# Optimization experiments

Measured on AMD Instinct MI355X. Metric: run time of the kernel, lower is better.

Reference implementation:

```python
import jax, jax.numpy as jnp
import numpy as np

B, A, NB, BOND = 256, 100, 10, 110
AF, BF, H, DEPTH = 82, 6, 300, 3

def setup_inputs() -> dict:
    key = jax.random.key(0)
    ks = jax.random.split(key, 16)
    atom_feats = jax.random.normal(ks[0], (B, A, AF), dtype=jnp.float32)
    bond_feats = jax.random.normal(ks[1], (B, BOND, BF), dtype=jnp.float32)
    ag_b = jax.random.randint(ks[2], (B, A, NB, 1), 0, B, dtype=jnp.int32)
    ag_a = jax.random.randint(ks[3], (B, A, NB, 1), 0, A, dtype=jnp.int32)
    atom_graph = jnp.concatenate([ag_b, ag_a], axis=-1)
    bg_b = jax.random.randint(ks[4], (B, A, NB, 1), 0, B, dtype=jnp.int32)
    bg_e = jax.random.randint(ks[5], (B, A, NB, 1), 0, BOND, dtype=jnp.int32)
    bond_graph = jnp.concatenate([bg_b, bg_e], axis=-1)
    num_nbs = jax.random.randint(ks[6], (B, A), 0, NB + 1, dtype=jnp.int32)
    n_atoms = jax.random.randint(ks[7], (B,), 50, A + 1, dtype=jnp.int32)
    n_atoms = n_atoms.at[0].set(A)  # padding must equal n_atoms.max()
    sc = lambda i, o: (2.0 / (i + o)) ** 0.5
    w_fc1 = jax.random.normal(ks[8], (AF, H), dtype=jnp.float32) * sc(AF, H)
    w_nei = jax.random.normal(ks[9], (H + BF, H), dtype=jnp.float32) * sc(H + BF, H)
    b_nei = jnp.zeros((H,), dtype=jnp.float32)
    w_atom = jax.random.normal(ks[10], (2 * H, H), dtype=jnp.float32) * sc(2 * H, H)
    b_atom = jnp.zeros((H,), dtype=jnp.float32)
    w2a = jax.random.normal(ks[11], (H, H), dtype=jnp.float32) * sc(H, H)
    w2b = jax.random.normal(ks[12], (BF, H), dtype=jnp.float32) * sc(BF, H)
    w_fc2 = jax.random.normal(ks[13], (H, H), dtype=jnp.float32) * sc(H, H)
    return dict(atom_feats=atom_feats, bond_feats=bond_feats, w_fc1=w_fc1,
                w_nei=w_nei, b_nei=b_nei, w_atom=w_atom, b_atom=b_atom,
                w2a=w2a, w2b=w2b, w_fc2=w_fc2, atom_graph=atom_graph,
                bond_graph=bond_graph, num_nbs=num_nbs, n_atoms=n_atoms)

def reference(atom_feats, bond_feats, w_fc1, w_nei, b_nei, w_atom, b_atom,
              w2a, w2b, w_fc2, atom_graph, bond_graph, num_nbs, n_atoms):
    h = jax.nn.relu(atom_feats @ w_fc1)                      # [B,A,H]
    bondnei = bond_feats[bond_graph[..., 0], bond_graph[..., 1]]  # [B,A,NB,BF]
    mask_neis = (num_nbs[..., None] > jnp.arange(NB, dtype=jnp.int32))[..., None]
    mask_atoms = (n_atoms[:, None] > jnp.arange(A, dtype=jnp.int32))[..., None]
    for i in range(DEPTH):
        atomnei = h[atom_graph[..., 0], atom_graph[..., 1]]  # [B,A,NB,H]
        if i + 1 == DEPTH:
            nei = (atomnei @ w2a) * (bondnei @ w2b)          # [B,A,NB,H]
            nei = jnp.where(mask_neis, nei, 0.0).sum(-2)     # [B,A,H]
            local = (h @ w_fc2) * nei
            local = jnp.where(mask_atoms, local, 0.0)
        else:
            nei = jax.nn.relu(jnp.concatenate([atomnei, bondnei], -1) @ w_nei + b_nei)
            nei = jnp.where(mask_neis, nei, 0.0).sum(-2)
            h = jax.nn.relu(jnp.concatenate([h, nei], -1) @ w_atom + b_atom)
    return local
```

## Files before the change

kernel.cpp:

```cpp
#include <hip/hip_runtime.h>

#define B_    256
#define A_    100
#define NB_   10
#define BOND_ 110
#define AF_   82
#define BF_   6
#define H_    300
#define NP_   320
#define MA_   (B_ * A_)
#define MB_   (B_ * BOND_)
#define KP300 320
#define KP82  96

typedef __attribute__((ext_vector_type(8))) short short8;
typedef __attribute__((ext_vector_type(4))) float f32x4;

__device__ __forceinline__ ushort f2bf(float v) {
    union { float f; unsigned u; } x; x.f = v;
    unsigned r = x.u + 0x7fffu + ((x.u >> 16) & 1u);
    return (ushort)(r >> 16);
}
__device__ __forceinline__ float bf2f(ushort h) {
    union { float f; unsigned u; } x; x.u = ((unsigned)h) << 16;
    return x.f;
}

__device__ __forceinline__ void gload16(const void* g, void* l) {
    __builtin_amdgcn_global_load_lds(
        (const __attribute__((address_space(1))) void*)g,
        (__attribute__((address_space(3))) void*)l, 16, 0, 0);
}

template<bool DUAL, bool BIAS, bool RELU, int OUTMODE>
__global__ __launch_bounds__(256, 2) void mgemm_k(
    const ushort* __restrict__ aH, const ushort* __restrict__ aL,
    const ushort* __restrict__ fH, const ushort* __restrict__ fL,
    const ushort* __restrict__ aH2, const ushort* __restrict__ aL2,
    const ushort* __restrict__ fH2, const ushort* __restrict__ fL2,
    int KP,
    const float* __restrict__ bias,
    const float* __restrict__ E,
    const int*   __restrict__ n_atoms,
    ushort* __restrict__ oHi, ushort* __restrict__ oLo,
    float*  __restrict__ oF)
{
    __shared__ char lds[3 * 8192];
    const int tid  = threadIdx.x;
    const int lane = tid & 63;
    const int l16  = lane & 15;
    const int kg   = lane >> 4;
    const int w    = tid >> 6;
    const int rowbase = blockIdx.x * 64;

    const int nks   = KP >> 5;
    const int total = (DUAL ? 2 : 1) * nks;

    const size_t srow = (size_t)(rowbase + (tid >> 2)) * KP;
    const int    sch  = (tid & 3) * 8;

    auto stage = [&](int t) {
        int pass = (DUAL && t >= nks) ? 1 : 0;
        int ks   = t - (pass ? nks : 0);
        const ushort* SH = pass ? aH2 : aH;
        const ushort* SL = pass ? aL2 : aL;
        char* dst = (char*)lds + (t % 3) * 8192 + (tid & 192) * 16;
        gload16(SH + srow + ks * 32 + sch, dst);
        gload16(SL + srow + ks * 32 + sch, dst + 4096);
    };

    f32x4 acc[4][5] = {};
    const int aoff = l16 * 64 + kg * 16;

    stage(0);
    for (int tk = 0; tk < total; ++tk) {
        short8 bh[5], bl[5];
        {
            int pass = (DUAL && tk >= nks) ? 1 : 0;
            int ks   = tk - (pass ? nks : 0);
            const ushort* FHp = pass ? fH2 : fH;
            const ushort* FLp = pass ? fL2 : fL;
            size_t base = ((size_t)ks * 20 + w * 5) * 512 + (size_t)lane * 8;
            #pragma unroll
            for (int c = 0; c < 5; ++c) {
                bh[c] = *(const short8*)(FHp + base + c * 512);
                bl[c] = *(const short8*)(FLp + base + c * 512);
            }
        }
        if (tk + 1 < total) stage(tk + 1);

        if (tk + 1 < total) { asm volatile("s_waitcnt vmcnt(2)" ::: "memory"); }
        else                { asm volatile("s_waitcnt vmcnt(0)" ::: "memory"); }
        __builtin_amdgcn_s_barrier();
        __builtin_amdgcn_sched_barrier(0);

        const char* ab = (const char*)lds + (tk % 3) * 8192;
        #pragma unroll
        for (int rt = 0; rt < 4; ++rt) {
            short8 ah = *(const short8*)(ab +        rt * 1024 + aoff);
            short8 al = *(const short8*)(ab + 4096 + rt * 1024 + aoff);
            #pragma unroll
            for (int c = 0; c < 5; ++c) {
                acc[rt][c] = __builtin_amdgcn_mfma_f32_16x16x32_bf16(ah, bh[c], acc[rt][c], 0, 0, 0);
                acc[rt][c] = __builtin_amdgcn_mfma_f32_16x16x32_bf16(al, bh[c], acc[rt][c], 0, 0, 0);
                acc[rt][c] = __builtin_amdgcn_mfma_f32_16x16x32_bf16(ah, bl[c], acc[rt][c], 0, 0, 0);
            }
        }
    }

    float biasv[5];
    #pragma unroll
    for (int c = 0; c < 5; ++c) {
        int col = w * 80 + c * 16 + l16;
        biasv[c] = (BIAS && col < H_) ? bias[col] : 0.f;
    }
    #pragma unroll
    for (int rt = 0; rt < 4; ++rt) {
        #pragma unroll
        for (int c = 0; c < 5; ++c) {
            const int col = w * 80 + c * 16 + l16;
            #pragma unroll
            for (int r = 0; r < 4; ++r) {
                const int row = rowbase + rt * 16 + kg * 4 + r;
                float v = acc[rt][c][r];
                if (BIAS) v += biasv[c];
                if (RELU) v = fmaxf(v, 0.f);
                if (OUTMODE == 0) {
                    ushort hi = f2bf(v);
                    ushort lo = f2bf(v - bf2f(hi));
                    size_t o = (size_t)row * NP_ + col;
                    oHi[o] = hi; oLo[o] = lo;
                } else if (OUTMODE == 1) {
                    oF[(size_t)row * NP_ + col] = v;
                } else {
                    if (col < H_) {
                        v *= E[(size_t)row * NP_ + col];
                        int b = row / A_;
                        int a = row - b * A_;
                        if (a >= n_atoms[b]) v = 0.f;
                        oF[(size_t)row * H_ + col] = v;
                    }
                }
            }
        }
    }
}

__global__ __launch_bounds__(256) void conv_wfrag_k(
    const float* __restrict__ src, int K, int KP,
    ushort* __restrict__ dH, ushort* __restrict__ dL)
{
    int idx = blockIdx.x * 256 + threadIdx.x;
    int nwords = (KP >> 5) * 20 * 64;
    if (idx >= nwords) return;
    int lane = idx & 63;
    int t  = idx >> 6;
    int ct = t % 20;
    int ks = t / 20;
    int col = ct * 16 + (lane & 15);
    int k0  = ks * 32 + (lane >> 4) * 8;
    short8 hv, lv;
    #pragma unroll
    for (int j = 0; j < 8; ++j) {
        int k = k0 + j;
        float v = (col < H_ && k < K) ? src[(size_t)k * H_ + col] : 0.f;
        ushort h = f2bf(v);
        hv[j] = (short)h;
        lv[j] = (short)f2bf(v - bf2f(h));
    }
    *(short8*)(dH + (size_t)idx * 8) = hv;
    *(short8*)(dL + (size_t)idx * 8) = lv;
}

__global__ __launch_bounds__(256) void conv_af_k(
    const float* __restrict__ src, ushort* __restrict__ dhi, ushort* __restrict__ dlo)
{
    int idx = blockIdx.x * 256 + threadIdx.x;
    if (idx >= MA_ * KP82) return;
    int row = idx / KP82, k = idx - row * KP82;
    float v = (k < AF_) ? src[(size_t)row * AF_ + k] : 0.f;
    ushort hi = f2bf(v);
    dhi[idx] = hi;
    dlo[idx] = f2bf(v - bf2f(hi));
}

__global__ __launch_bounds__(256) void bondmm_k(
    const float* __restrict__ bf, const float* __restrict__ wmat,
    const float* __restrict__ bias, float* __restrict__ out)
{
    int idx = blockIdx.x * 256 + threadIdx.x;
    if (idx >= MB_ * 80) return;
    int row = idx / 80, c4 = idx - row * 80;
    float4 s = make_float4(0.f, 0.f, 0.f, 0.f);
    if (c4 < 75) {
        int col = c4 * 4;
        if (bias) s = *(const float4*)(bias + col);
        #pragma unroll
        for (int k = 0; k < 6; ++k) {
            float b = bf[(size_t)row * 6 + k];
            float4 wv = *(const float4*)(wmat + (size_t)k * H_ + col);
            s.x = fmaf(b, wv.x, s.x); s.y = fmaf(b, wv.y, s.y);
            s.z = fmaf(b, wv.z, s.z); s.w = fmaf(b, wv.w, s.w);
        }
    }
    *(float4*)(out + (size_t)row * NP_ + c4 * 4) = s;
}

__global__ __launch_bounds__(256) void agg_relu_k(
    const float* __restrict__ hw, const float* __restrict__ bwn,
    const int* __restrict__ ag, const int* __restrict__ bg,
    const int* __restrict__ num_nbs,
    ushort* __restrict__ neiH, ushort* __restrict__ neiL)
{
    int idx = blockIdx.x * 256 + threadIdx.x;
    if (idx >= MA_ * 80) return;
    int ba = idx / 80, c4 = idx - ba * 80;
    int nn = num_nbs[ba];
    const int* agp = ag + (size_t)ba * NB_ * 2;
    const int* bgp = bg + (size_t)ba * NB_ * 2;
    float4 s = make_float4(0.f, 0.f, 0.f, 0.f);
    for (int n = 0; n < nn; ++n) {
        int arow = agp[2*n] * A_    + agp[2*n+1];
        int brow = bgp[2*n] * BOND_ + bgp[2*n+1];
        float4 hv = *(const float4*)(hw  + (size_t)arow * NP_ + c4 * 4);
        float4 bv = *(const float4*)(bwn + (size_t)brow * NP_ + c4 * 4);
        s.x += fmaxf(hv.x + bv.x, 0.f); s.y += fmaxf(hv.y + bv.y, 0.f);
        s.z += fmaxf(hv.z + bv.z, 0.f); s.w += fmaxf(hv.w + bv.w, 0.f);
    }
    size_t o = (size_t)ba * NP_ + c4 * 4;
    ushort4 hi, lo;
    hi.x = f2bf(s.x); lo.x = f2bf(s.x - bf2f(hi.x));
    hi.y = f2bf(s.y); lo.y = f2bf(s.y - bf2f(hi.y));
    hi.z = f2bf(s.z); lo.z = f2bf(s.z - bf2f(hi.z));
    hi.w = f2bf(s.w); lo.w = f2bf(s.w - bf2f(hi.w));
    *(ushort4*)(neiH + o) = hi;
    *(ushort4*)(neiL + o) = lo;
}

__global__ __launch_bounds__(256) void agg_prod_k(
    const float* __restrict__ hw2, const float* __restrict__ bw2,
    const int* __restrict__ ag, const int* __restrict__ bg,
    const int* __restrict__ num_nbs, float* __restrict__ neiF)
{
    int idx = blockIdx.x * 256 + threadIdx.x;
    if (idx >= MA_ * 80) return;
    int ba = idx / 80, c4 = idx - ba * 80;
    int nn = num_nbs[ba];
    const int* agp = ag + (size_t)ba * NB_ * 2;
    const int* bgp = bg + (size_t)ba * NB_ * 2;
    float4 s = make_float4(0.f, 0.f, 0.f, 0.f);
    for (int n = 0; n < nn; ++n) {
        int arow = agp[2*n] * A_    + agp[2*n+1];
        int brow = bgp[2*n] * BOND_ + bgp[2*n+1];
        float4 hv = *(const float4*)(hw2 + (size_t)arow * NP_ + c4 * 4);
        float4 bv = *(const float4*)(bw2 + (size_t)brow * NP_ + c4 * 4);
        s.x = fmaf(hv.x, bv.x, s.x); s.y = fmaf(hv.y, bv.y, s.y);
        s.z = fmaf(hv.z, bv.z, s.z); s.w = fmaf(hv.w, bv.w, s.w);
    }
    *(float4*)(neiF + (size_t)ba * NP_ + c4 * 4) = s;
}

extern "C" void kernel_launch(void* const* d_in, const int* in_sizes, int n_in,
                              void* d_out, int out_size, void* d_ws, size_t ws_size,
                              hipStream_t stream)
{
    const float* atom_feats = (const float*)d_in[0];
    const float* bond_feats = (const float*)d_in[1];
    const float* w_fc1      = (const float*)d_in[2];
    const float* w_nei      = (const float*)d_in[3];
    const float* b_nei      = (const float*)d_in[4];
    const float* w_atom     = (const float*)d_in[5];
    const float* b_atom     = (const float*)d_in[6];
    const float* w2a        = (const float*)d_in[7];
    const float* w2b        = (const float*)d_in[8];
    const float* w_fc2      = (const float*)d_in[9];
    const int*   atom_graph = (const int*)d_in[10];
    const int*   bond_graph = (const int*)d_in[11];
    const int*   num_nbs    = (const int*)d_in[12];
    const int*   n_atoms    = (const int*)d_in[13];
    float* out = (float*)d_out;
    (void)in_sizes; (void)n_in; (void)out_size; (void)ws_size;

    const size_t SZ_H16 = (size_t)MA_ * NP_ * 2;
    const size_t SZ_HF  = (size_t)MA_ * NP_ * 4;
    const size_t SZ_BWN = (size_t)MB_ * NP_ * 4;
    const size_t SZ_AF  = (size_t)MA_ * KP82 * 2;
    const size_t SZ_WT  = (size_t)NP_ * KP300 * 2;
    const size_t SZ_WT1 = (size_t)NP_ * KP82 * 2;
    char* p = (char*)d_ws;
    ushort* hA_h = (ushort*)p; p += SZ_H16;
    ushort* hA_l = (ushort*)p; p += SZ_H16;
    ushort* hB_h = (ushort*)p; p += SZ_H16;
    ushort* hB_l = (ushort*)p; p += SZ_H16;
    ushort* nei_h = (ushort*)p; p += SZ_H16;
    ushort* nei_l = (ushort*)p; p += SZ_H16;
    float* hwF = (float*)p; p += SZ_HF;
    float* bwn = (float*)p; p += SZ_BWN;
    ushort* af_h = (ushort*)p; p += SZ_AF;
    ushort* af_l = (ushort*)p; p += SZ_AF;
    ushort* wfc1_h = (ushort*)p; p += SZ_WT1;
    ushort* wfc1_l = (ushort*)p; p += SZ_WT1;
    ushort* wn1_h  = (ushort*)p; p += SZ_WT;
    ushort* wn1_l  = (ushort*)p; p += SZ_WT;
    ushort* wa1_h  = (ushort*)p; p += SZ_WT;
    ushort* wa1_l  = (ushort*)p; p += SZ_WT;
    ushort* wa2_h  = (ushort*)p; p += SZ_WT;
    ushort* wa2_l  = (ushort*)p; p += SZ_WT;
    ushort* w2a_h  = (ushort*)p; p += SZ_WT;
    ushort* w2a_l  = (ushort*)p; p += SZ_WT;
    ushort* wfc2_h = (ushort*)p; p += SZ_WT;
    ushort* wfc2_l = (ushort*)p; p += SZ_WT;
    float* neiF = (float*)hB_h;

    const dim3 blk(256);
    const dim3 gG(MA_ / 64);
    const int  aggG  = (MA_ * 80 + 255) / 256;
    const int  bondG = (MB_ * 80 + 255) / 256;
    const int  fw300 = ((KP300 >> 5) * 20 * 64 + 255) / 256;
    const int  fw96  = ((KP82  >> 5) * 20 * 64 + 255) / 256;

    conv_af_k<<<(MA_*KP82+255)/256, blk, 0, stream>>>(atom_feats, af_h, af_l);
    conv_wfrag_k<<<fw96,  blk, 0, stream>>>(w_fc1, AF_, KP82, wfc1_h, wfc1_l);
    conv_wfrag_k<<<fw300, blk, 0, stream>>>(w_nei,                 H_, KP300, wn1_h, wn1_l);
    conv_wfrag_k<<<fw300, blk, 0, stream>>>(w_atom,                H_, KP300, wa1_h, wa1_l);
    conv_wfrag_k<<<fw300, blk, 0, stream>>>(w_atom + (size_t)H_*H_, H_, KP300, wa2_h, wa2_l);
    conv_wfrag_k<<<fw300, blk, 0, stream>>>(w2a,                   H_, KP300, w2a_h, w2a_l);
    conv_wfrag_k<<<fw300, blk, 0, stream>>>(w_fc2,                 H_, KP300, wfc2_h, wfc2_l);

    bondmm_k<<<bondG, blk, 0, stream>>>(bond_feats, w_nei + (size_t)H_*H_, b_nei, bwn);

    mgemm_k<false,false,true,0><<<gG, blk, 0, stream>>>(
        af_h, af_l, wfc1_h, wfc1_l, nullptr,nullptr,nullptr,nullptr, KP82,
        nullptr, nullptr, nullptr, hA_h, hA_l, nullptr);

    ushort* hc_h = hA_h; ushort* hc_l = hA_l;
    ushort* hn_h = hB_h; ushort* hn_l = hB_l;
    for (int it = 0; it < 2; ++it) {
        mgemm_k<false,false,false,1><<<gG, blk, 0, stream>>>(
            hc_h, hc_l, wn1_h, wn1_l, nullptr,nullptr,nullptr,nullptr, KP300,
            nullptr, nullptr, nullptr, nullptr, nullptr, hwF);
        agg_relu_k<<<aggG, blk, 0, stream>>>(hwF, bwn, atom_graph, bond_graph, num_nbs, nei_h, nei_l);
        mgemm_k<true,true,true,0><<<gG, blk, 0, stream>>>(
            hc_h, hc_l, wa1_h, wa1_l, nei_h, nei_l, wa2_h, wa2_l, KP300,
            b_atom, nullptr, nullptr, hn_h, hn_l, nullptr);
        ushort* t;
        t = hc_h; hc_h = hn_h; hn_h = t;
        t = hc_l; hc_l = hn_l; hn_l = t;
    }

    bondmm_k<<<bondG, blk, 0, stream>>>(bond_feats, w2b, nullptr, bwn);
    mgemm_k<false,false,false,1><<<gG, blk, 0, stream>>>(
        hc_h, hc_l, w2a_h, w2a_l, nullptr,nullptr,nullptr,nullptr, KP300,
        nullptr, nullptr, nullptr, nullptr, nullptr, hwF);
    agg_prod_k<<<aggG, blk, 0, stream>>>(hwF, bwn, atom_graph, bond_graph, num_nbs, neiF);
    mgemm_k<false,false,false,2><<<gG, blk, 0, stream>>>(
        hc_h, hc_l, wfc2_h, wfc2_l, nullptr,nullptr,nullptr,nullptr, KP300,
        nullptr, neiF, n_atoms, nullptr, nullptr, out);
}
```

Baseline: 454.5 us.

## Enlarge GEMM row tile to 100 rows with 512-thread blocks and 4-stage pipeline

The bf16-split GEMM kernel now uses 512-thread blocks covering 100 rows (one molecule) per block. Eight waves are arranged as 2 row groups by 4 column groups, and the second row group handles only 3 row tiles. The A-tile staging becomes a 4-buffer LDS ring with double-buffered B fragments in registers and a two-step unrolled loop with explicit vmcnt waits, so weight fragment loads are reused across more rows and overlapped with MFMA work. The grid shrinks to 256 blocks. This risks lower occupancy from higher register and LDS use, and wastes work on padded row tiles.

```diff
diff --git a/kernel.cpp b/kernel.cpp
--- a/kernel.cpp
+++ b/kernel.cpp
@@ -13,6 +13,12 @@
 #define KP300 320
 #define KP82  96
 
+#define BM_     100
+#define BMST_   112
+#define PLANE_  7168
+#define BUFSZ_  14336
+#define DUMP_   57344
+
 typedef __attribute__((ext_vector_type(8))) short short8;
 typedef __attribute__((ext_vector_type(4))) float f32x4;
 
@@ -33,7 +39,7 @@
 }
 
 template<bool DUAL, bool BIAS, bool RELU, int OUTMODE>
-__global__ __launch_bounds__(256, 2) void mgemm_k(
+__global__ __launch_bounds__(512, 2) void mgemm_k(
     const ushort* __restrict__ aH, const ushort* __restrict__ aL,
     const ushort* __restrict__ fH, const ushort* __restrict__ fL,
     const ushort* __restrict__ aH2, const ushort* __restrict__ aL2,
@@ -45,100 +51,162 @@
     ushort* __restrict__ oHi, ushort* __restrict__ oLo,
     float*  __restrict__ oF)
 {
-    __shared__ char lds[3 * 8192];
+    __shared__ char lds[4 * BUFSZ_ + 2048];
     const int tid  = threadIdx.x;
     const int lane = tid & 63;
     const int l16  = lane & 15;
     const int kg   = lane >> 4;
     const int w    = tid >> 6;
-    const int rowbase = blockIdx.x * 64;
+    const int wr   = w >> 2;
+    const int wc   = w & 3;
+    const int nrt  = wr ? 3 : 4;
+    const int rowbase = blockIdx.x * BM_;
 
     const int nks   = KP >> 5;
     const int total = (DUAL ? 2 : 1) * nks;
 
-    const size_t srow = (size_t)(rowbase + (tid >> 2)) * KP;
-    const int    sch  = (tid & 3) * 8;
+    bool  spl[2], sdmp[2];
+    size_t ssoff[2];
+    int   sdoff[2];
+    #pragma unroll
+    for (int i = 0; i < 2; ++i) {
+        int s = 2 * w + i;
+        bool isdump = (s >= 14);
+        int se = isdump ? 0 : s;
+        int p  = (se >= 7) ? 1 : 0;
+        int t  = se - p * 7;
+        int row = t * 16 + (lane >> 2);
+        int grow = rowbase + row; if (grow >= MA_) grow = MA_ - 1;
+        spl[i]  = (p != 0);
+        sdmp[i] = isdump;
+        ssoff[i] = (size_t)grow * KP + (lane & 3) * 8;
+        sdoff[i] = isdump ? (DUMP_ + i * 1024) : (p * PLANE_ + t * 1024);
+    }
 
     auto stage = [&](int t) {
         int pass = (DUAL && t >= nks) ? 1 : 0;
         int ks   = t - (pass ? nks : 0);
-        const ushort* SH = pass ? aH2 : aH;
-        const ushort* SL = pass ? aL2 : aL;
-        char* dst = (char*)lds + (t % 3) * 8192 + (tid & 192) * 16;
-        gload16(SH + srow + ks * 32 + sch, dst);
-        gload16(SL + srow + ks * 32 + sch, dst + 4096);
+        const ushort* PH = pass ? aH2 : aH;
+        const ushort* PL = pass ? aL2 : aL;
+        char* bb = (char*)lds + (t & 3) * BUFSZ_;
+        #pragma unroll
+        for (int i = 0; i < 2; ++i) {
+            const ushort* src = (spl[i] ? PL : PH) + ssoff[i] + ks * 32;
+            char* dst = (sdmp[i] ? (char*)lds : bb) + sdoff[i];
+            gload16(src, dst);
+        }
     };
 
+    auto loadB = [&](int t, short8* bh, short8* bl) {
+        int pass = (DUAL && t >= nks) ? 1 : 0;
+        int ks   = t - (pass ? nks : 0);
+        const ushort* FHp = pass ? fH2 : fH;
+        const ushort* FLp = pass ? fL2 : fL;
+        size_t base = ((size_t)ks * 20 + wc * 5) * 512 + (size_t)lane * 8;
+        #pragma unroll
+        for (int c = 0; c < 5; ++c) {
+            bh[c] = *(const short8*)(FHp + base + c * 512);
+            bl[c] = *(const short8*)(FLp + base + c * 512);
+        }
+    };
+
     f32x4 acc[4][5] = {};
-    const int aoff = l16 * 64 + kg * 16;
+    const int ao = l16 * 64 + kg * 16;
+
+    auto mstep = [&](int t, const short8* bh, const short8* bl) {
+        const char* ab = (const char*)lds + (t & 3) * BUFSZ_ + wr * 4096;
+        #pragma unroll
+        for (int rt = 0; rt < 4; ++rt) {
+            if (rt < nrt) {
+                short8 ah = *(const short8*)(ab + rt * 1024 + ao);
+                short8 al = *(const short8*)(ab + PLANE_ + rt * 1024 + ao);
+                #pragma unroll
+                for (int c = 0; c < 5; ++c) {
+                    acc[rt][c] = __builtin_amdgcn_mfma_f32_16x16x32_bf16(ah, bh[c], acc[rt][c], 0, 0, 0);
+                    acc[rt][c] = __builtin_amdgcn_mfma_f32_16x16x32_bf16(al, bh[c], acc[rt][c], 0, 0, 0);
+                    acc[rt][c] = __builtin_amdgcn_mfma_f32_16x16x32_bf16(ah, bl[c], acc[rt][c], 0, 0, 0);
+                }
+            }
+        }
+    };
+
+    short8 bAh[5], bAl[5], bBh[5], bBl[5];
 
     stage(0);
-    for (int tk = 0; tk < total; ++tk) {
-        short8 bh[5], bl[5];
-        {
-            int pass = (DUAL && tk >= nks) ? 1 : 0;
-            int ks   = tk - (pass ? nks : 0);
-            const ushort* FHp = pass ? fH2 : fH;
-            const ushort* FLp = pass ? fL2 : fL;
-            size_t base = ((size_t)ks * 20 + w * 5) * 512 + (size_t)lane * 8;
-            #pragma unroll
-            for (int c = 0; c < 5; ++c) {
-                bh[c] = *(const short8*)(FHp + base + c * 512);
-                bl[c] = *(const short8*)(FLp + base + c * 512);
-            }
-        }
-        if (tk + 1 < total) stage(tk + 1);
-
-        if (tk + 1 < total) { asm volatile("s_waitcnt vmcnt(2)" ::: "memory"); }
-        else                { asm volatile("s_waitcnt vmcnt(0)" ::: "memory"); }
+    __builtin_amdgcn_sched_barrier(0);
+    loadB(0, bAh, bAl);
+    __builtin_amdgcn_sched_barrier(0);
+    if (1 < total) stage(1);
+    __builtin_amdgcn_sched_barrier(0);
+
+    for (int tk = 0; tk < total; tk += 2) {
+        if (tk + 2 < total) {
+            loadB(tk + 1, bBh, bBl);
+            __builtin_amdgcn_sched_barrier(0);
+            stage(tk + 2);
+            asm volatile("s_waitcnt vmcnt(14)" ::: "memory");
+        } else if (tk + 1 < total) {
+            loadB(tk + 1, bBh, bBl);
+            asm volatile("s_waitcnt vmcnt(12)" ::: "memory");
+        } else {
+            asm volatile("s_waitcnt vmcnt(0)" ::: "memory");
+        }
         __builtin_amdgcn_s_barrier();
         __builtin_amdgcn_sched_barrier(0);
-
-        const char* ab = (const char*)lds + (tk % 3) * 8192;
-        #pragma unroll
-        for (int rt = 0; rt < 4; ++rt) {
-            short8 ah = *(const short8*)(ab +        rt * 1024 + aoff);
-            short8 al = *(const short8*)(ab + 4096 + rt * 1024 + aoff);
-            #pragma unroll
-            for (int c = 0; c < 5; ++c) {
-                acc[rt][c] = __builtin_amdgcn_mfma_f32_16x16x32_bf16(ah, bh[c], acc[rt][c], 0, 0, 0);
-                acc[rt][c] = __builtin_amdgcn_mfma_f32_16x16x32_bf16(al, bh[c], acc[rt][c], 0, 0, 0);
-                acc[rt][c] = __builtin_amdgcn_mfma_f32_16x16x32_bf16(ah, bl[c], acc[rt][c], 0, 0, 0);
-            }
-        }
+        mstep(tk, bAh, bAl);
+        if (tk + 1 >= total) break;
+
+        if (tk + 3 < total) {
+            loadB(tk + 2, bAh, bAl);
+            __builtin_amdgcn_sched_barrier(0);
+            stage(tk + 3);
+            asm volatile("s_waitcnt vmcnt(14)" ::: "memory");
+        } else if (tk + 2 < total) {
+            loadB(tk + 2, bAh, bAl);
+            asm volatile("s_waitcnt vmcnt(12)" ::: "memory");
+        } else {
+            asm volatile("s_waitcnt vmcnt(0)" ::: "memory");
+        }
+        __builtin_amdgcn_s_barrier();
+        __builtin_amdgcn_sched_barrier(0);
+        mstep(tk + 1, bBh, bBl);
     }
 
     float biasv[5];
     #pragma unroll
     for (int c = 0; c < 5; ++c) {
-        int col = w * 80 + c * 16 + l16;
+        int col = wc * 80 + c * 16 + l16;
         biasv[c] = (BIAS && col < H_) ? bias[col] : 0.f;
     }
     #pragma unroll
     for (int rt = 0; rt < 4; ++rt) {
-        #pragma unroll
-        for (int c = 0; c < 5; ++c) {
-            const int col = w * 80 + c * 16 + l16;
+        if (rt < nrt) {
             #pragma unroll
-            for (int r = 0; r < 4; ++r) {
-                const int row = rowbase + rt * 16 + kg * 4 + r;
-                float v = acc[rt][c][r];
-                if (BIAS) v += biasv[c];
-                if (RELU) v = fmaxf(v, 0.f);
-                if (OUTMODE == 0) {
-                    ushort hi = f2bf(v);
-                    ushort lo = f2bf(v - bf2f(hi));
-                    size_t o = (size_t)row * NP_ + col;
-                    oHi[o] = hi; oLo[o] = lo;
-                } else if (OUTMODE == 1) {
-                    oF[(size_t)row * NP_ + col] = v;
-                } else {
-                    if (col < H_) {
-                        v *= E[(size_t)row * NP_ + col];
-                        int b = row / A_;
-                        int a = row - b * A_;
-                        if (a >= n_atoms[b]) v = 0.f;
-                        oF[(size_t)row * H_ + col] = v;
+            for (int c = 0; c < 5; ++c) {
+                const int col = wc * 80 + c * 16 + l16;
+                #pragma unroll
+                for (int r = 0; r < 4; ++r) {
+                    const int lrow = wr * 64 + rt * 16 + kg * 4 + r;
+                    if (lrow >= BM_) continue;
+                    const int row = rowbase + lrow;
+                    float v = acc[rt][c][r];
+                    if (BIAS) v += biasv[c];
+                    if (RELU) v = fmaxf(v, 0.f);
+                    if (OUTMODE == 0) {
+                        ushort hi = f2bf(v);
+                        ushort lo = f2bf(v - bf2f(hi));
+                        size_t o = (size_t)row * NP_ + col;
+                        oHi[o] = hi; oLo[o] = lo;
+                    } else if (OUTMODE == 1) {
+                        oF[(size_t)row * NP_ + col] = v;
+                    } else {
+                        if (col < H_) {
+                            v *= E[(size_t)row * NP_ + col];
+                            int b = row / A_;
+                            int a = row - b * A_;
+                            if (a >= n_atoms[b]) v = 0.f;
+                            oF[(size_t)row * H_ + col] = v;
+                        }
                     }
                 }
             }
@@ -313,7 +381,8 @@
     float* neiF = (float*)hB_h;
 
     const dim3 blk(256);
-    const dim3 gG(MA_ / 64);
+    const dim3 blkG(512);
+    const dim3 gG(B_);
     const int  aggG  = (MA_ * 80 + 255) / 256;
     const int  bondG = (MB_ * 80 + 255) / 256;
     const int  fw300 = ((KP300 >> 5) * 20 * 64 + 255) / 256;
@@ -329,18 +398,18 @@
 
     bondmm_k<<<bondG, blk, 0, stream>>>(bond_feats, w_nei + (size_t)H_*H_, b_nei, bwn);
 
-    mgemm_k<false,false,true,0><<<gG, blk, 0, stream>>>(
+    mgemm_k<false,false,true,0><<<gG, blkG, 0, stream>>>(
         af_h, af_l, wfc1_h, wfc1_l, nullptr,nullptr,nullptr,nullptr, KP82,
         nullptr, nullptr, nullptr, hA_h, hA_l, nullptr);
 
     ushort* hc_h = hA_h; ushort* hc_l = hA_l;
     ushort* hn_h = hB_h; ushort* hn_l = hB_l;
     for (int it = 0; it < 2; ++it) {
-        mgemm_k<false,false,false,1><<<gG, blk, 0, stream>>>(
+        mgemm_k<false,false,false,1><<<gG, blkG, 0, stream>>>(
             hc_h, hc_l, wn1_h, wn1_l, nullptr,nullptr,nullptr,nullptr, KP300,
             nullptr, nullptr, nullptr, nullptr, nullptr, hwF);
         agg_relu_k<<<aggG, blk, 0, stream>>>(hwF, bwn, atom_graph, bond_graph, num_nbs, nei_h, nei_l);
-        mgemm_k<true,true,true,0><<<gG, blk, 0, stream>>>(
+        mgemm_k<true,true,true,0><<<gG, blkG, 0, stream>>>(
             hc_h, hc_l, wa1_h, wa1_l, nei_h, nei_l, wa2_h, wa2_l, KP300,
             b_atom, nullptr, nullptr, hn_h, hn_l, nullptr);
         ushort* t;
@@ -349,11 +418,11 @@
     }
 
     bondmm_k<<<bondG, blk, 0, stream>>>(bond_feats, w2b, nullptr, bwn);
-    mgemm_k<false,false,false,1><<<gG, blk, 0, stream>>>(
+    mgemm_k<false,false,false,1><<<gG, blkG, 0, stream>>>(
         hc_h, hc_l, w2a_h, w2a_l, nullptr,nullptr,nullptr,nullptr, KP300,
         nullptr, nullptr, nullptr, nullptr, nullptr, hwF);
     agg_prod_k<<<aggG, blk, 0, stream>>>(hwF, bwn, atom_graph, bond_graph, num_nbs, neiF);
-    mgemm_k<false,false,false,2><<<gG, blk, 0, stream>>>(
+    mgemm_k<false,false,false,2><<<gG, blkG, 0, stream>>>(
         hc_h, hc_l, wfc2_h, wfc2_l, nullptr,nullptr,nullptr,nullptr, KP300,
         nullptr, neiF, n_atoms, nullptr, nullptr, out);
 }
```

After: 619.6 us. 36.3% more time.

## Double-buffer B-fragment loads and prefetch LDS A tiles two stages ahead

Applied to the files above, without the earlier changes.

Restructures the GEMM main loop into a two-step unrolled software pipeline. B fragments now go into alternating register sets and are loaded one step ahead, and the A tiles are staged into LDS two steps ahead using the triple buffer. The goal is to hide global-load latency for the weights behind the MFMA work instead of waiting on them each iteration. In exchange it holds twice as many B registers, which may reduce occupancy, and it relies on hand-tuned vmcnt counts.

```diff
diff --git a/kernel.cpp b/kernel.cpp
--- a/kernel.cpp
+++ b/kernel.cpp
@@ -69,32 +69,24 @@
         gload16(SL + srow + ks * 32 + sch, dst + 4096);
     };
 
+    auto loadB = [&](int t, short8* bh, short8* bl) {
+        int pass = (DUAL && t >= nks) ? 1 : 0;
+        int ks   = t - (pass ? nks : 0);
+        const ushort* FHp = pass ? fH2 : fH;
+        const ushort* FLp = pass ? fL2 : fL;
+        size_t base = ((size_t)ks * 20 + w * 5) * 512 + (size_t)lane * 8;
+        #pragma unroll
+        for (int c = 0; c < 5; ++c) {
+            bh[c] = *(const short8*)(FHp + base + c * 512);
+            bl[c] = *(const short8*)(FLp + base + c * 512);
+        }
+    };
+
     f32x4 acc[4][5] = {};
     const int aoff = l16 * 64 + kg * 16;
 
-    stage(0);
-    for (int tk = 0; tk < total; ++tk) {
-        short8 bh[5], bl[5];
-        {
-            int pass = (DUAL && tk >= nks) ? 1 : 0;
-            int ks   = tk - (pass ? nks : 0);
-            const ushort* FHp = pass ? fH2 : fH;
-            const ushort* FLp = pass ? fL2 : fL;
-            size_t base = ((size_t)ks * 20 + w * 5) * 512 + (size_t)lane * 8;
-            #pragma unroll
-            for (int c = 0; c < 5; ++c) {
-                bh[c] = *(const short8*)(FHp + base + c * 512);
-                bl[c] = *(const short8*)(FLp + base + c * 512);
-            }
-        }
-        if (tk + 1 < total) stage(tk + 1);
-
-        if (tk + 1 < total) { asm volatile("s_waitcnt vmcnt(2)" ::: "memory"); }
-        else                { asm volatile("s_waitcnt vmcnt(0)" ::: "memory"); }
-        __builtin_amdgcn_s_barrier();
-        __builtin_amdgcn_sched_barrier(0);
-
-        const char* ab = (const char*)lds + (tk % 3) * 8192;
+    auto mstep = [&](int t, const short8* bh, const short8* bl) {
+        const char* ab = (const char*)lds + (t % 3) * 8192;
         #pragma unroll
         for (int rt = 0; rt < 4; ++rt) {
             short8 ah = *(const short8*)(ab +        rt * 1024 + aoff);
@@ -106,6 +98,40 @@
                 acc[rt][c] = __builtin_amdgcn_mfma_f32_16x16x32_bf16(ah, bl[c], acc[rt][c], 0, 0, 0);
             }
         }
+    };
+
+    short8 bAh[5], bAl[5], bBh[5], bBl[5];
+
+    stage(0);
+    __builtin_amdgcn_sched_barrier(0);
+    loadB(0, bAh, bAl);
+    __builtin_amdgcn_sched_barrier(0);
+    if (1 < total) stage(1);
+    __builtin_amdgcn_sched_barrier(0);
+
+    for (int tk = 0; tk < total; tk += 2) {
+        if (tk + 1 < total) {
+            loadB(tk + 1, bBh, bBl);
+            asm volatile("s_waitcnt vmcnt(12)" ::: "memory");
+        } else {
+            asm volatile("s_waitcnt vmcnt(0)" ::: "memory");
+        }
+        __builtin_amdgcn_s_barrier();
+        __builtin_amdgcn_sched_barrier(0);
+        if (tk + 2 < total) stage(tk + 2);
+        mstep(tk, bAh, bAl);
+        if (tk + 1 >= total) break;
+
+        if (tk + 2 < total) {
+            loadB(tk + 2, bAh, bAl);
+            asm volatile("s_waitcnt vmcnt(12)" ::: "memory");
+        } else {
+            asm volatile("s_waitcnt vmcnt(0)" ::: "memory");
+        }
+        __builtin_amdgcn_s_barrier();
+        __builtin_amdgcn_sched_barrier(0);
+        if (tk + 3 < total) stage(tk + 3);
+        mstep(tk + 1, bBh, bBl);
     }
 
     float biasv[5];
```

New measurement: 509.0 us. +12.0%, slower.

## Halve GEMM row tile to 32 and merge weight conversion kernels into one launch

Applied to the files above, without the earlier changes.

The split-bf16 GEMM kernel now processes 32 rows per block instead of 64. This halves the accumulator registers and LDS staging, and launch bounds are raised to allow 4 blocks per CU. Each thread now stages one 16-byte load per step (half the threads load hi, half lo) instead of two, so the wait count changes accordingly. Separately, the six weight-fragment conversion launches are fused into one kernel that picks its weight matrix from the block index, cutting launch overhead. The smaller tile doubles the grid for more parallelism and occupancy, at the cost of reloading the B fragments from global memory twice as often.

```diff
diff --git a/kernel.cpp b/kernel.cpp
--- a/kernel.cpp
+++ b/kernel.cpp
@@ -33,7 +33,7 @@
 }
 
 template<bool DUAL, bool BIAS, bool RELU, int OUTMODE>
-__global__ __launch_bounds__(256, 2) void mgemm_k(
+__global__ __launch_bounds__(256, 4) void mgemm_k(
     const ushort* __restrict__ aH, const ushort* __restrict__ aL,
     const ushort* __restrict__ fH, const ushort* __restrict__ fL,
     const ushort* __restrict__ aH2, const ushort* __restrict__ aL2,
@@ -45,31 +45,30 @@
     ushort* __restrict__ oHi, ushort* __restrict__ oLo,
     float*  __restrict__ oF)
 {
-    __shared__ char lds[3 * 8192];
+    __shared__ char lds[3 * 4096];
     const int tid  = threadIdx.x;
     const int lane = tid & 63;
     const int l16  = lane & 15;
     const int kg   = lane >> 4;
     const int w    = tid >> 6;
-    const int rowbase = blockIdx.x * 64;
+    const int rowbase = blockIdx.x * 32;
 
     const int nks   = KP >> 5;
     const int total = (DUAL ? 2 : 1) * nks;
 
-    const size_t srow = (size_t)(rowbase + (tid >> 2)) * KP;
+    const int    spl  = tid >> 7;
+    const size_t srow = (size_t)(rowbase + ((tid & 127) >> 2)) * KP;
     const int    sch  = (tid & 3) * 8;
+    const int    sdst = spl * 2048 + (tid & 127) * 16;
 
     auto stage = [&](int t) {
         int pass = (DUAL && t >= nks) ? 1 : 0;
         int ks   = t - (pass ? nks : 0);
-        const ushort* SH = pass ? aH2 : aH;
-        const ushort* SL = pass ? aL2 : aL;
-        char* dst = (char*)lds + (t % 3) * 8192 + (tid & 192) * 16;
-        gload16(SH + srow + ks * 32 + sch, dst);
-        gload16(SL + srow + ks * 32 + sch, dst + 4096);
+        const ushort* S = (pass ? (spl ? aL2 : aH2) : (spl ? aL : aH));
+        gload16(S + srow + ks * 32 + sch, (char*)lds + (t % 3) * 4096 + sdst);
     };
 
-    f32x4 acc[4][5] = {};
+    f32x4 acc[2][5] = {};
     const int aoff = l16 * 64 + kg * 16;
 
     stage(0);
@@ -89,16 +88,16 @@
         }
         if (tk + 1 < total) stage(tk + 1);
 
-        if (tk + 1 < total) { asm volatile("s_waitcnt vmcnt(2)" ::: "memory"); }
+        if (tk + 1 < total) { asm volatile("s_waitcnt vmcnt(1)" ::: "memory"); }
         else                { asm volatile("s_waitcnt vmcnt(0)" ::: "memory"); }
         __builtin_amdgcn_s_barrier();
         __builtin_amdgcn_sched_barrier(0);
 
-        const char* ab = (const char*)lds + (tk % 3) * 8192;
+        const char* ab = (const char*)lds + (tk % 3) * 4096;
         #pragma unroll
-        for (int rt = 0; rt < 4; ++rt) {
+        for (int rt = 0; rt < 2; ++rt) {
             short8 ah = *(const short8*)(ab +        rt * 1024 + aoff);
-            short8 al = *(const short8*)(ab + 4096 + rt * 1024 + aoff);
+            short8 al = *(const short8*)(ab + 2048 + rt * 1024 + aoff);
             #pragma unroll
             for (int c = 0; c < 5; ++c) {
                 acc[rt][c] = __builtin_amdgcn_mfma_f32_16x16x32_bf16(ah, bh[c], acc[rt][c], 0, 0, 0);
@@ -115,7 +114,7 @@
         biasv[c] = (BIAS && col < H_) ? bias[col] : 0.f;
     }
     #pragma unroll
-    for (int rt = 0; rt < 4; ++rt) {
+    for (int rt = 0; rt < 2; ++rt) {
         #pragma unroll
         for (int c = 0; c < 5; ++c) {
             const int col = w * 80 + c * 16 + l16;
@@ -146,17 +145,39 @@
     }
 }
 
-__global__ __launch_bounds__(256) void conv_wfrag_k(
-    const float* __restrict__ src, int K, int KP,
-    ushort* __restrict__ dH, ushort* __restrict__ dL)
-{
-    int idx = blockIdx.x * 256 + threadIdx.x;
-    int nwords = (KP >> 5) * 20 * 64;
-    if (idx >= nwords) return;
+__global__ __launch_bounds__(256) void conv_wall_k(
+    const float* __restrict__ w_fc1, const float* __restrict__ w_nei,
+    const float* __restrict__ w_atom, const float* __restrict__ w2a,
+    const float* __restrict__ w_fc2,
+    ushort* __restrict__ wfc1_h, ushort* __restrict__ wfc1_l,
+    ushort* __restrict__ wn1_h,  ushort* __restrict__ wn1_l,
+    ushort* __restrict__ wa1_h,  ushort* __restrict__ wa1_l,
+    ushort* __restrict__ wa2_h,  ushort* __restrict__ wa2_l,
+    ushort* __restrict__ w2a_h,  ushort* __restrict__ w2a_l,
+    ushort* __restrict__ wfc2_h, ushort* __restrict__ wfc2_l)
+{
+    const int b = blockIdx.x;
+    const float* src; int K; ushort *dH, *dL; int idx;
+    if (b < 15) {
+        src = w_fc1; K = AF_; dH = wfc1_h; dL = wfc1_l;
+        idx = b * 256 + threadIdx.x;
+        if (idx >= (KP82 >> 5) * 20 * 64) return;
+    } else {
+        int t = (b - 15) / 50, rb = (b - 15) % 50;
+        K = H_;
+        switch (t) {
+            case 0: src = w_nei;                    dH = wn1_h;  dL = wn1_l;  break;
+            case 1: src = w_atom;                   dH = wa1_h;  dL = wa1_l;  break;
+            case 2: src = w_atom + (size_t)H_ * H_; dH = wa2_h;  dL = wa2_l;  break;
+            case 3: src = w2a;                      dH = w2a_h;  dL = w2a_l;  break;
+            default: src = w_fc2;                   dH = wfc2_h; dL = wfc2_l; break;
+        }
+        idx = rb * 256 + threadIdx.x;
+    }
     int lane = idx & 63;
-    int t  = idx >> 6;
-    int ct = t % 20;
-    int ks = t / 20;
+    int t2 = idx >> 6;
+    int ct = t2 % 20;
+    int ks = t2 / 20;
     int col = ct * 16 + (lane & 15);
     int k0  = ks * 32 + (lane >> 4) * 8;
     short8 hv, lv;
@@ -313,19 +334,16 @@
     float* neiF = (float*)hB_h;
 
     const dim3 blk(256);
-    const dim3 gG(MA_ / 64);
+    const dim3 gG(MA_ / 32);
     const int  aggG  = (MA_ * 80 + 255) / 256;
     const int  bondG = (MB_ * 80 + 255) / 256;
-    const int  fw300 = ((KP300 >> 5) * 20 * 64 + 255) / 256;
-    const int  fw96  = ((KP82  >> 5) * 20 * 64 + 255) / 256;
+    const int  wallG = 15 + 5 * 50;
 
     conv_af_k<<<(MA_*KP82+255)/256, blk, 0, stream>>>(atom_feats, af_h, af_l);
-    conv_wfrag_k<<<fw96,  blk, 0, stream>>>(w_fc1, AF_, KP82, wfc1_h, wfc1_l);
-    conv_wfrag_k<<<fw300, blk, 0, stream>>>(w_nei,                 H_, KP300, wn1_h, wn1_l);
-    conv_wfrag_k<<<fw300, blk, 0, stream>>>(w_atom,                H_, KP300, wa1_h, wa1_l);
-    conv_wfrag_k<<<fw300, blk, 0, stream>>>(w_atom + (size_t)H_*H_, H_, KP300, wa2_h, wa2_l);
-    conv_wfrag_k<<<fw300, blk, 0, stream>>>(w2a,                   H_, KP300, w2a_h, w2a_l);
-    conv_wfrag_k<<<fw300, blk, 0, stream>>>(w_fc2,                 H_, KP300, wfc2_h, wfc2_l);
+    conv_wall_k<<<wallG, blk, 0, stream>>>(
+        w_fc1, w_nei, w_atom, w2a, w_fc2,
+        wfc1_h, wfc1_l, wn1_h, wn1_l, wa1_h, wa1_l,
+        wa2_h, wa2_l, w2a_h, w2a_l, wfc2_h, wfc2_l);
 
     bondmm_k<<<bondG, blk, 0, stream>>>(bond_feats, w_nei + (size_t)H_*H_, b_nei, bwn);
 
```

Result: slower. 498.6 us (+9.7%).
